# Kernel tuning notes

Hardware: AMD Instinct MI355X
Metric: run time of the kernel (lower is better)

Reference implementation:

```python
import jax, jax.numpy as jnp
import numpy as np

HID = 4096      # hidden_size
H = 32          # num_attention_heads
K = 8           # num_key_value_heads
D = HID // H    # head_dim = 128
G = H // K      # q heads per kv group = 4
INTER = 14336   # intermediate_size
T = 2048        # tokens (prefill)
EPS = 1e-5
THETA = 1000000.0


def setup_inputs() -> dict:
    key = jax.random.key(0)
    ks = jax.random.split(key, 9)
    s = 0.02
    return {
        "hidden_states": jax.random.normal(ks[0], (T, HID), jnp.float32),
        "position_ids": jnp.arange(T, dtype=jnp.int64),
        "wqkv": jax.random.normal(ks[1], ((H + 2 * K) * D, HID), jnp.float32) * s,
        "wo": jax.random.normal(ks[2], (HID, HID), jnp.float32) * s,
        "w1": jax.random.normal(ks[3], (INTER, HID), jnp.float32) * s,  # gate
        "w3": jax.random.normal(ks[4], (INTER, HID), jnp.float32) * s,  # up
        "w2": jax.random.normal(ks[5], (HID, INTER), jnp.float32) * s,  # down
        "attn_norm_w": jnp.ones((HID,), jnp.float32),
        "ffn_norm_w": jnp.ones((HID,), jnp.float32),
    }


def _rmsnorm(x, w):
    var = jnp.mean(jnp.square(x), axis=-1, keepdims=True)
    return x * jax.lax.rsqrt(var + EPS) * w


def _rope(x, cos, sin):
    # non-interleaved (half-split) rotation; x: [T, h, D], cos/sin: [T, 1, D//2]
    x1, x2 = x[..., : D // 2], x[..., D // 2 :]
    return jnp.concatenate([x1 * cos - x2 * sin, x2 * cos + x1 * sin], axis=-1)


def _attention(x, position_ids, wqkv, wo):
    t = x.shape[0]
    qkv = x @ wqkv.T  # [T, (H+2K)*D]
    q = qkv[:, : H * D].reshape(t, H, D)
    k = qkv[:, H * D : (H + K) * D].reshape(t, K, D)
    v = qkv[:, (H + K) * D :].reshape(t, K, D)

    inv_freq = 1.0 / (THETA ** (jnp.arange(0, D, 2, dtype=jnp.float32) / D))
    freqs = position_ids.astype(jnp.float32)[:, None] * inv_freq  # [T, D//2]
    cos = jnp.cos(freqs)[:, None, :]
    sin = jnp.sin(freqs)[:, None, :]
    q = _rope(q, cos, sin)
    k = _rope(k, cos, sin)

    # grouped-query attention: [T, K, G, D] queries vs [T, K, D] keys
    qg = q.reshape(t, K, G, D)
    scale = 1.0 / jnp.sqrt(jnp.float32(D))
    scores = jnp.einsum("tkgd,skd->kgts", qg, k) * scale  # [K, G, T, T]
    causal = jnp.tril(jnp.ones((t, t), dtype=bool))
    scores = jnp.where(causal, scores, jnp.finfo(scores.dtype).min)
    probs = jax.nn.softmax(scores, axis=-1)
    out = jnp.einsum("kgts,skd->tkgd", probs, v).reshape(t, H * D)
    return out @ wo.T


def _mlp(x, w1, w3, w2):
    return (jax.nn.silu(x @ w1.T) * (x @ w3.T)) @ w2.T


def reference(hidden_states, position_ids, wqkv, wo, w1, w3, w2, attn_norm_w, ffn_norm_w):
    h = hidden_states + _attention(_rmsnorm(hidden_states, attn_norm_w), position_ids, wqkv, wo)
    return h + _mlp(_rmsnorm(h, ffn_norm_w), w1, w3, w2)
```

## Files before the change

kernel.cpp:

```cpp
#include <hip/hip_runtime.h>
#include <stdint.h>

#define T_SEQ 2048
#define HIDN  4096
#define NH    32
#define NKV   8
#define DH    128
#define INTER 14336
#define QKV_N 6144
#define EPSR  1e-5f
#define SCALE 0.08838834764831845f
#define KVB   64

typedef __bf16 bf16x8 __attribute__((ext_vector_type(8)));
typedef float  f32x4  __attribute__((ext_vector_type(4)));

__device__ __forceinline__ f32x4 mfma16(bf16x8 a, bf16x8 b, f32x4 c) {
  return __builtin_amdgcn_mfma_f32_16x16x32_bf16(a, b, c, 0, 0, 0);
}

__device__ __forceinline__ void glds16(const void* g, void* l) {
  __builtin_amdgcn_global_load_lds(
      (__attribute__((address_space(1))) void*)g,
      (__attribute__((address_space(3))) void*)l,
      16, 0, 0);
}

__global__ __launch_bounds__(256) void cvt_all_kernel(
    const float* __restrict__ wqkv, const float* __restrict__ wo,
    const float* __restrict__ w1, const float* __restrict__ w3,
    const float* __restrict__ w2, __bf16* __restrict__ dst) {
  const long E0 = (long)QKV_N * HIDN;
  const long E1 = E0 + (long)HIDN * HIDN;
  const long E2 = E1 + 2L * INTER * HIDN;
  const long E3 = E2 + (long)HIDN * INTER;
  long stride = (long)gridDim.x * 256 * 16;
  for (long f = ((long)blockIdx.x * 256 + threadIdx.x) * 16; f < E3; f += stride) {
    const float* src;
    if (f < E0) {
      src = wqkv + f;
    } else if (f < E1) {
      src = wo + (f - E0);
    } else if (f < E2) {
      long l = f - E1;
      int c = (int)(l >> 12), i = (int)(l & 4095);
      int tau = c >> 8, j2 = c & 255;
      int wn = j2 >> 6, j = j2 & 63, nt = j >> 4, k16 = j & 15;
      src = (nt < 2 ? w1 : w3) +
            (size_t)(tau * 128 + wn * 32 + (nt & 1) * 16 + k16) * HIDN + i;
    } else {
      src = w2 + (f - E2);
    }
    float4 a = *(const float4*)(src);
    float4 b = *(const float4*)(src + 4);
    float4 e = *(const float4*)(src + 8);
    float4 g = *(const float4*)(src + 12);
    bf16x8 o0, o1;
    o0[0]=(__bf16)a.x; o0[1]=(__bf16)a.y; o0[2]=(__bf16)a.z; o0[3]=(__bf16)a.w;
    o0[4]=(__bf16)b.x; o0[5]=(__bf16)b.y; o0[6]=(__bf16)b.z; o0[7]=(__bf16)b.w;
    o1[0]=(__bf16)e.x; o1[1]=(__bf16)e.y; o1[2]=(__bf16)e.z; o1[3]=(__bf16)e.w;
    o1[4]=(__bf16)g.x; o1[5]=(__bf16)g.y; o1[6]=(__bf16)g.z; o1[7]=(__bf16)g.w;
    *(bf16x8*)(dst + f) = o0;
    *(bf16x8*)(dst + f + 8) = o1;
  }
}

__global__ __launch_bounds__(256) void rmsnorm_kernel(
    const float* __restrict__ x, const float* __restrict__ w,
    __bf16* __restrict__ y) {
  const int row = blockIdx.x, tid = threadIdx.x;
  const float* xr = x + (size_t)row * HIDN + tid * 16;
  float4 v0 = ((const float4*)xr)[0];
  float4 v1 = ((const float4*)xr)[1];
  float4 v2 = ((const float4*)xr)[2];
  float4 v3 = ((const float4*)xr)[3];
  float ss = v0.x*v0.x + v0.y*v0.y + v0.z*v0.z + v0.w*v0.w
           + v1.x*v1.x + v1.y*v1.y + v1.z*v1.z + v1.w*v1.w
           + v2.x*v2.x + v2.y*v2.y + v2.z*v2.z + v2.w*v2.w
           + v3.x*v3.x + v3.y*v3.y + v3.z*v3.z + v3.w*v3.w;
  #pragma unroll
  for (int off = 32; off >= 1; off >>= 1) ss += __shfl_xor(ss, off, 64);
  __shared__ float red[4];
  if ((tid & 63) == 0) red[tid >> 6] = ss;
  __syncthreads();
  float rn = rsqrtf((red[0] + red[1] + red[2] + red[3]) * (1.0f / HIDN) + EPSR);
  const float* wr = w + tid * 16;
  #pragma unroll
  for (int h = 0; h < 2; h++) {
    float4 a = ((const float4*)xr)[h*2], b = ((const float4*)xr)[h*2+1];
    float4 wa = ((const float4*)wr)[h*2], wb = ((const float4*)wr)[h*2+1];
    bf16x8 o;
    o[0]=(__bf16)(a.x*rn*wa.x); o[1]=(__bf16)(a.y*rn*wa.y);
    o[2]=(__bf16)(a.z*rn*wa.z); o[3]=(__bf16)(a.w*rn*wa.w);
    o[4]=(__bf16)(b.x*rn*wb.x); o[5]=(__bf16)(b.y*rn*wb.y);
    o[6]=(__bf16)(b.z*rn*wb.z); o[7]=(__bf16)(b.w*rn*wb.w);
    *(bf16x8*)(y + (size_t)row * HIDN + tid * 16 + h * 8) = o;
  }
}

__global__ __launch_bounds__(256) void add3_rms_kernel(
    const float* __restrict__ p, const float* __restrict__ resid,
    const float* __restrict__ w, float* __restrict__ hout,
    __bf16* __restrict__ xn) {
  const int row = blockIdx.x, tid = threadIdx.x;
  const size_t base = (size_t)row * HIDN + tid * 16;
  const size_t half = (size_t)T_SEQ * HIDN;
  float h[16];
  float ss = 0.f;
  #pragma unroll
  for (int q = 0; q < 4; q++) {
    float4 a = *(const float4*)(p + base + q * 4);
    float4 b = *(const float4*)(p + half + base + q * 4);
    float4 c = *(const float4*)(resid + base + q * 4);
    h[q*4+0] = a.x + b.x + c.x; h[q*4+1] = a.y + b.y + c.y;
    h[q*4+2] = a.z + b.z + c.z; h[q*4+3] = a.w + b.w + c.w;
    ss += h[q*4]*h[q*4] + h[q*4+1]*h[q*4+1] + h[q*4+2]*h[q*4+2] + h[q*4+3]*h[q*4+3];
    *(float4*)(hout + base + q * 4) = *(float4*)&h[q*4];
  }
  #pragma unroll
  for (int off = 32; off >= 1; off >>= 1) ss += __shfl_xor(ss, off, 64);
  __shared__ float red[4];
  if ((tid & 63) == 0) red[tid >> 6] = ss;
  __syncthreads();
  float rn = rsqrtf((red[0] + red[1] + red[2] + red[3]) * (1.0f / HIDN) + EPSR);
  #pragma unroll
  for (int hb = 0; hb < 2; hb++) {
    bf16x8 o;
    #pragma unroll
    for (int e = 0; e < 8; e++) {
      float wv = w[tid * 16 + hb * 8 + e];
      o[e] = (__bf16)(h[hb*8+e] * rn * wv);
    }
    *(bf16x8*)(xn + base + hb * 8) = o;
  }
}

template<int EPI>
__global__ __launch_bounds__(512, 2) void gemm256_kernel(
    const __bf16* __restrict__ A, const __bf16* __restrict__ B,
    void* __restrict__ Cout, int M, int N, int Kfull, int KZ, int Nout) {
  extern __shared__ __align__(16) char smem[];
  const int tid = threadIdx.x;
  const int lane = tid & 63;
  const int wv = tid >> 6;
  const int wm = wv >> 2;
  const int wn = wv & 3;
  const int lr = lane & 15, ql = lane >> 4;

  const int gx = gridDim.x, gy = gridDim.y;
  const int nwg = gx * gy;
  const int orig = blockIdx.y * gx + blockIdx.x;
  const int cpx = nwg >> 3;
  const int swz = (orig & 7) * cpx + (orig >> 3);
  const int by = swz % gy, bx = swz / gy;
  const int m0 = by * 256, n0 = bx * 256;
  const int kbase = blockIdx.z * KZ;
  const int NT = KZ >> 6;

  const int u0 = tid, u1 = tid + 512;
  const int r0 = u0 >> 2, r1 = u1 >> 2;
  const int p0 = (u0 & 3) ^ ((r0 >> 1) & 3);
  const int p1 = (u1 & 3) ^ ((r1 >> 1) & 3);
  const char* aR0 = (const char*)(A + (size_t)(m0 + r0) * Kfull + kbase) + p0 * 16;
  const char* aR1 = (const char*)(A + (size_t)(m0 + r1) * Kfull + kbase) + p1 * 16;
  const char* bR0 = (const char*)(B + (size_t)(n0 + r0) * Kfull + kbase) + p0 * 16;
  const char* bR1 = (const char*)(B + (size_t)(n0 + r1) * Kfull + kbase) + p1 * 16;
  const int d0 = u0 * 16, d1 = u1 * 16;

  const int sA = ql ^ ((lr >> 1) & 3);
  int aoff[8], boff[4];
  #pragma unroll
  for (int mt = 0; mt < 8; mt++) aoff[mt] = (wm * 128 + mt * 16 + lr) * 64 + sA * 16;
  #pragma unroll
  for (int nt = 0; nt < 4; nt++) boff[nt] = (wn * 64 + nt * 16 + lr) * 64 + sA * 16;

#define STAGE_A(t, kh, b) do {                                         \
    const size_t _o = (size_t)(t) * 128 + (kh) * 64;                   \
    glds16(aR0 + _o, smem + (b) * 65536 + (kh) * 16384 + d0);          \
    glds16(aR1 + _o, smem + (b) * 65536 + (kh) * 16384 + d1);          \
  } while (0)
#define STAGE_B(t, kh, b) do {                                         \
    const size_t _o = (size_t)(t) * 128 + (kh) * 64;                   \
    glds16(bR0 + _o, smem + (b) * 65536 + 32768 + (kh) * 16384 + d0);  \
    glds16(bR1 + _o, smem + (b) * 65536 + 32768 + (kh) * 16384 + d1);  \
  } while (0)
#define LDA4(dst, mb, b, ks) do {                                      \
    const char* _p = smem + (b) * 65536 + (ks) * 16384;                \
    dst[0] = *(const bf16x8*)(_p + aoff[(mb) + 0]);                    \
    dst[1] = *(const bf16x8*)(_p + aoff[(mb) + 1]);                    \
    dst[2] = *(const bf16x8*)(_p + aoff[(mb) + 2]);                    \
    dst[3] = *(const bf16x8*)(_p + aoff[(mb) + 3]);                    \
  } while (0)
#define LDB4(dst, b, ks) do {                                          \
    const char* _p = smem + (b) * 65536 + 32768 + (ks) * 16384;        \
    dst[0] = *(const bf16x8*)(_p + boff[0]);                           \
    dst[1] = *(const bf16x8*)(_p + boff[1]);                           \
    dst[2] = *(const bf16x8*)(_p + boff[2]);                           \
    dst[3] = *(const bf16x8*)(_p + boff[3]);                           \
  } while (0)
#define VMW(n)  asm volatile("s_waitcnt vmcnt(" #n ")" ::: "memory")
#define BAR()   __builtin_amdgcn_s_barrier()
#define LGKM(n) do { asm volatile("s_waitcnt lgkmcnt(" #n ")" ::: "memory"); \
    __builtin_amdgcn_sched_barrier(0); } while (0)
#define MFMA16(mb, AF, BF) do {                                        \
    __builtin_amdgcn_s_setprio(1);                                     \
    _Pragma("unroll") for (int _m = 0; _m < 4; _m++)                   \
      _Pragma("unroll") for (int _n = 0; _n < 4; _n++)                 \
        acc[(mb) + _m][_n] = mfma16(AF[_m], BF[_n], acc[(mb) + _m][_n]); \
    __builtin_amdgcn_s_setprio(0);                                     \
  } while (0)

  f32x4 acc[8][4] = {};
  bf16x8 af0[4], af1[4], bf0[4], bf1[4];

  STAGE_A(0, 0, 0); STAGE_B(0, 0, 0);
  STAGE_A(0, 1, 0); STAGE_B(0, 1, 0);
  STAGE_A(1, 0, 1); STAGE_B(1, 0, 1);
  VMW(8);
  BAR();
  LDA4(af0, 0, 0, 0); LDB4(bf0, 0, 0);

  const int NI = NT >> 1;
  for (int i = 0; i < NI - 1; ++i) {
    const int t1 = 2 * i + 1, s2 = 2 * i + 2, s3 = 2 * i + 3;
    LDA4(af1, 4, 0, 0);
    STAGE_A(t1, 1, 1);
    LGKM(4);
    MFMA16(0, af0, bf0);
    VMW(6); BAR();
    LDA4(af0, 0, 0, 1); LDB4(bf1, 0, 1);
    STAGE_B(t1, 1, 1);
    LGKM(8);
    MFMA16(4, af1, bf0);
    VMW(6); BAR();
    LDA4(af1, 4, 0, 1);
    STAGE_A(s2, 0, 0);
    LGKM(4);
    MFMA16(0, af0, bf1);
    VMW(6); BAR();
    LDA4(af0, 0, 1, 0); LDB4(bf0, 1, 0);
    STAGE_B(s2, 0, 0);
    LGKM(8);
    MFMA16(4, af1, bf1);
    VMW(6); BAR();
    LDA4(af1, 4, 1, 0);
    STAGE_A(s2, 1, 0);
    LGKM(4);
    MFMA16(0, af0, bf0);
    VMW(6); BAR();
    LDA4(af0, 0, 1, 1); LDB4(bf1, 1, 1);
    STAGE_B(s2, 1, 0);
    LGKM(8);
    MFMA16(4, af1, bf0);
    VMW(6); BAR();
    LDA4(af1, 4, 1, 1);
    STAGE_A(s3, 0, 1);
    LGKM(4);
    MFMA16(0, af0, bf1);
    VMW(6); BAR();
    LDA4(af0, 0, 0, 0); LDB4(bf0, 0, 0);
    STAGE_B(s3, 0, 1);
    LGKM(8);
    MFMA16(4, af1, bf1);
    VMW(6); BAR();
  }
  {
    const int t1 = NT - 1;
    LDA4(af1, 4, 0, 0);
    STAGE_A(t1, 1, 1);
    LGKM(4);
    MFMA16(0, af0, bf0);
    VMW(6); BAR();
    LDA4(af0, 0, 0, 1); LDB4(bf1, 0, 1);
    STAGE_B(t1, 1, 1);
    LGKM(8);
    MFMA16(4, af1, bf0);
    BAR();
    LDA4(af1, 4, 0, 1);
    LGKM(4);
    MFMA16(0, af0, bf1);
    VMW(2); BAR();
    LDA4(af0, 0, 1, 0); LDB4(bf0, 1, 0);
    LGKM(8);
    MFMA16(4, af1, bf1);
    BAR();
    LDA4(af1, 4, 1, 0);
    LGKM(4);
    MFMA16(0, af0, bf0);
    VMW(0); BAR();
    LDA4(af0, 0, 1, 1); LDB4(bf1, 1, 1);
    LGKM(8);
    MFMA16(4, af1, bf0);
    BAR();
    LDA4(af1, 4, 1, 1);
    LGKM(4);
    MFMA16(0, af0, bf1);
    BAR();
    LGKM(0);
    MFMA16(4, af1, bf1);
  }

#undef STAGE_A
#undef STAGE_B
#undef LDA4
#undef LDB4
#undef VMW
#undef BAR
#undef LGKM
#undef MFMA16

  #pragma unroll
  for (int mt = 0; mt < 8; mt++) {
    #pragma unroll
    for (int r = 0; r < 4; r++) {
      int rr = m0 + wm * 128 + mt * 16 + ql * 4 + r;
      if (EPI == 2) {
        #pragma unroll
        for (int nt = 0; nt < 2; nt++) {
          float u = acc[mt][nt][r];
          float v = acc[mt][nt + 2][r];
          float g = u / (1.0f + __expf(-u)) * v;
          int cc = (n0 >> 1) + wn * 32 + nt * 16 + lr;
          ((__bf16*)Cout)[(size_t)rr * Nout + cc] = (__bf16)g;
        }
      } else {
        #pragma unroll
        for (int nt = 0; nt < 4; nt++) {
          int cc = n0 + wn * 64 + nt * 16 + lr;
          size_t ix = (size_t)rr * N + cc;
          float val = acc[mt][nt][r];
          if (EPI == 0) ((float*)Cout)[(size_t)blockIdx.z * M * N + ix] = val;
          else          ((__bf16*)Cout)[ix] = (__bf16)val;
        }
      }
    }
  }
}

__global__ __launch_bounds__(256) void add3_kernel(
    const float* __restrict__ p, const float* __restrict__ r,
    float* __restrict__ o, long n) {
  long stride = (long)gridDim.x * 1024;
  for (long i = ((long)blockIdx.x * 256 + threadIdx.x) * 4; i < n; i += stride) {
    float4 a = *(const float4*)(p + i);
    float4 b = *(const float4*)(p + n + i);
    float4 c = *(const float4*)(r + i);
    float4 o4;
    o4.x = a.x + b.x + c.x; o4.y = a.y + b.y + c.y;
    o4.z = a.z + b.z + c.z; o4.w = a.w + b.w + c.w;
    *(float4*)(o + i) = o4;
  }
}

__global__ __launch_bounds__(256) void rope_vtrans_kernel(
    const __bf16* __restrict__ qkv, __bf16* __restrict__ q_r,
    __bf16* __restrict__ k_r, __bf16* __restrict__ v_t) {
  __shared__ float cs[64], sn[64];
  __shared__ __bf16 tile[64][136];
  const int tid = threadIdx.x;
  const int bid = blockIdx.x;
  if (bid < T_SEQ) {
    const int t = bid;
    if (tid < 64) {
      float inv = exp2f(-(float)tid * (19.931568569324174f / 64.0f));
      float f = (float)t * inv;
      cs[tid] = cosf(f);
      sn[tid] = sinf(f);
    }
    __syncthreads();
    const __bf16* row = qkv + (size_t)t * QKV_N;
    for (int it = tid; it < 40 * 64; it += 256) {
      int hh = it >> 6, i = it & 63;
      float x1 = (float)row[hh * 128 + i];
      float x2 = (float)row[hh * 128 + 64 + i];
      float c = cs[i], s = sn[i];
      float o1 = x1 * c - x2 * s;
      float o2 = x2 * c + x1 * s;
      if (hh < NH) {
        __bf16* qo = q_r + (size_t)t * HIDN + hh * 128;
        qo[i] = (__bf16)o1;
        qo[64 + i] = (__bf16)o2;
      } else {
        __bf16* ko = k_r + (size_t)t * (NKV * DH) + (hh - NH) * 128;
        ko[i] = (__bf16)o1;
        ko[64 + i] = (__bf16)o2;
      }
    }
  } else {
    const int b2 = bid - T_SEQ;
    const int t0 = (b2 & 31) * 64, kh = b2 >> 5;
    #pragma unroll
    for (int i = 0; i < 4; i++) {
      int u = i * 256 + tid;
      int row = u >> 4, c = (u & 15) * 8;
      *(bf16x8*)&tile[row][c] =
          *(const bf16x8*)(qkv + (size_t)(t0 + row) * QKV_N + (NH + NKV) * DH + kh * DH + c);
    }
    __syncthreads();
    const int d = tid & 127, th = (tid >> 7) * 32;
    #pragma unroll
    for (int j = 0; j < 4; j++) {
      int t = th + j * 8;
      bf16x8 o;
      #pragma unroll
      for (int e = 0; e < 8; e++) o[e] = tile[t + e][d];
      *(bf16x8*)(v_t + ((size_t)kh * DH + d) * T_SEQ + t0 + t) = o;
    }
  }
}

__global__ __launch_bounds__(256) void attn_kernel(
    const __bf16* __restrict__ q_r, const __bf16* __restrict__ k_r,
    const __bf16* __restrict__ v_t, __bf16* __restrict__ attn_o) {
  __shared__ __align__(16) __bf16 Ks[KVB * 128];
  __shared__ __align__(16) __bf16 Vs[128 * KVB];
  __shared__ __align__(16) __bf16 Pl[4 * 16 * KVB];

  const int tid = threadIdx.x;
  const int lane = tid & 63, wv = tid >> 6;
  const int lr = lane & 15, g = lane >> 4;
  const int qt = gridDim.x - 1 - blockIdx.x;
  const int h = blockIdx.y;
  const int kh = h >> 2;
  const int q0b = qt * 64;
  const int q0w = q0b + wv * 16;

  bf16x8 qf[4];
  {
    const __bf16* qp = q_r + (size_t)(q0w + lr) * HIDN + h * DH + g * 8;
    #pragma unroll
    for (int kk = 0; kk < 4; kk++) qf[kk] = *(const bf16x8*)(qp + kk * 32);
  }

  f32x4 o[8] = {};
  float mrun[4] = {-1e30f, -1e30f, -1e30f, -1e30f};
  float lrun[4] = {0.f, 0.f, 0.f, 0.f};
  char* PlW = (char*)Pl + wv * 2048;

  for (int kv0 = 0; kv0 < q0b + KVB; kv0 += KVB) {
    __syncthreads();
    #pragma unroll
    for (int i = 0; i < 4; i++) {
      int u = i * 256 + tid;
      int row = u >> 4;
      int cb = ((u & 15) * 16) ^ ((row & 7) << 4);
      glds16((const char*)(k_r + (size_t)(kv0 + row) * (NKV * DH) + kh * DH) + cb,
             (char*)Ks + u * 16);
    }
    #pragma unroll
    for (int i = 0; i < 4; i++) {
      int u = i * 256 + tid;
      int row = u >> 3;
      int cb = ((u & 7) * 16) ^ ((row & 7) << 4);
      glds16((const char*)(v_t + ((size_t)kh * DH + row) * T_SEQ + kv0) + cb,
             (char*)Vs + u * 16);
    }
    __syncthreads();

    if (q0w + 15 >= kv0) {
      f32x4 s[4] = {};
      #pragma unroll
      for (int kk = 0; kk < 4; kk++) {
        #pragma unroll
        for (int jt = 0; jt < 4; jt++) {
          int krow = jt * 16 + lr;
          int cb = (kk * 64 + g * 16) ^ ((krow & 7) << 4);
          bf16x8 kf = *(const bf16x8*)((char*)Ks + krow * 256 + cb);
          s[jt] = mfma16(qf[kk], kf, s[jt]);
        }
      }
      const bool need_mask = (kv0 + KVB - 1) > q0w;
      #pragma unroll
      for (int r = 0; r < 4; r++) {
        int qpos = q0w + g * 4 + r;
        int prow = g * 4 + r;
        float p[4];
        #pragma unroll
        for (int jt = 0; jt < 4; jt++) {
          float v = s[jt][r] * SCALE;
          if (need_mask && (kv0 + jt * 16 + lr > qpos)) v = -1e30f;
          p[jt] = v;
        }
        float mx = fmaxf(fmaxf(p[0], p[1]), fmaxf(p[2], p[3]));
        #pragma unroll
        for (int off = 1; off < 16; off <<= 1) mx = fmaxf(mx, __shfl_xor(mx, off, 64));
        float mn = fmaxf(mrun[r], mx);
        float corr = __expf(mrun[r] - mn);
        mrun[r] = mn;
        float ps = 0.f;
        #pragma unroll
        for (int jt = 0; jt < 4; jt++) {
          p[jt] = __expf(p[jt] - mn);
          ps += p[jt];
          int cbyte = ((jt * 16 + lr) * 2) ^ ((prow & 7) << 4);
          *(__bf16*)(PlW + prow * 128 + cbyte) = (__bf16)p[jt];
        }
        #pragma unroll
        for (int off = 1; off < 16; off <<= 1) ps += __shfl_xor(ps, off, 64);
        lrun[r] = lrun[r] * corr + ps;
        #pragma unroll
        for (int nt = 0; nt < 8; nt++) o[nt][r] *= corr;
      }
      bf16x8 pa[2];
      #pragma unroll
      for (int ks = 0; ks < 2; ks++)
        pa[ks] = *(const bf16x8*)(PlW + lr * 128 + ((g * 16 + ks * 64) ^ ((lr & 7) << 4)));
      #pragma unroll
      for (int nt = 0; nt < 8; nt++) {
        #pragma unroll
        for (int ks = 0; ks < 2; ks++) {
          int vrow = nt * 16 + lr;
          int cb = (ks * 64 + g * 16) ^ ((vrow & 7) << 4);
          bf16x8 vf = *(const bf16x8*)((char*)Vs + vrow * 128 + cb);
          o[nt] = mfma16(pa[ks], vf, o[nt]);
        }
      }
    }
  }

  #pragma unroll
  for (int nt = 0; nt < 8; nt++) {
    #pragma unroll
    for (int r = 0; r < 4; r++) {
      int qrow = q0w + g * 4 + r;
      int d = nt * 16 + lr;
      attn_o[(size_t)qrow * HIDN + h * DH + d] = (__bf16)(o[nt][r] / lrun[r]);
    }
  }
}

extern "C" void kernel_launch(void* const* d_in, const int* in_sizes, int n_in,
                              void* d_out, int out_size, void* d_ws, size_t ws_size,
                              hipStream_t stream) {
  const float* hidden = (const float*)d_in[0];
  const float* wqkv = (const float*)d_in[2];
  const float* wo   = (const float*)d_in[3];
  const float* w1   = (const float*)d_in[4];
  const float* w3   = (const float*)d_in[5];
  const float* w2   = (const float*)d_in[6];
  const float* anw  = (const float*)d_in[7];
  const float* fnw  = (const float*)d_in[8];

  char* ws = (char*)d_ws;
  const size_t SZ_XN   = (size_t)T_SEQ * HIDN * 2;
  const size_t SZ_QKV  = (size_t)T_SEQ * QKV_N * 2;
  const size_t SZ_KR   = (size_t)T_SEQ * NKV * DH * 2;
  const size_t SZ_H    = (size_t)T_SEQ * HIDN * 4;
  const size_t SZ_UV   = (size_t)T_SEQ * INTER * 2;

  const size_t W_QKV = (size_t)QKV_N * HIDN * 2;
  const size_t W_O   = (size_t)HIDN * HIDN * 2;
  const size_t W_I   = (size_t)INTER * HIDN * 2;
  const size_t W_TOTAL = W_QKV + W_O + 3 * W_I;

  char* act = ws + W_TOTAL;

  __bf16* xn1    = (__bf16*)(act);
  __bf16* qkv    = (__bf16*)(act + SZ_XN);
  __bf16* q_r    = (__bf16*)(act + SZ_XN + SZ_QKV);
  __bf16* gbuf   = (__bf16*)(act);
  __bf16* k_r    = (__bf16*)(act + SZ_UV);
  __bf16* attn_o = (__bf16*)(act + SZ_UV + SZ_KR);
  float*  hbuf   = (float*) (act + SZ_UV + SZ_KR + SZ_XN);
  __bf16* v_t    = (__bf16*)(act + SZ_UV + SZ_KR + SZ_XN);
  __bf16* xn2    = (__bf16*)(act + SZ_UV + SZ_KR + SZ_XN + SZ_H);
  float*  pbuf   = (float*)(act + SZ_UV + SZ_KR + SZ_XN + SZ_H + SZ_XN);

  __bf16* wall_b = (__bf16*)(ws);
  __bf16* wqkv_b = wall_b;
  __bf16* wo_b   = (__bf16*)(ws + W_QKV);
  __bf16* w13_b  = (__bf16*)(ws + W_QKV + W_O);
  __bf16* w2_b   = (__bf16*)(ws + W_QKV + W_O + 2 * W_I);

  const int LDS_BYTES = 131072;
  hipFuncSetAttribute((const void*)gemm256_kernel<0>,
                      hipFuncAttributeMaxDynamicSharedMemorySize, LDS_BYTES);
  hipFuncSetAttribute((const void*)gemm256_kernel<1>,
                      hipFuncAttributeMaxDynamicSharedMemorySize, LDS_BYTES);
  hipFuncSetAttribute((const void*)gemm256_kernel<2>,
                      hipFuncAttributeMaxDynamicSharedMemorySize, LDS_BYTES);

  cvt_all_kernel<<<2048, 256, 0, stream>>>(wqkv, wo, w1, w3, w2, wall_b);

  rmsnorm_kernel<<<T_SEQ, 256, 0, stream>>>(hidden, anw, xn1);
  gemm256_kernel<1><<<dim3(QKV_N / 256, T_SEQ / 256, 1), 512, LDS_BYTES, stream>>>(
      xn1, wqkv_b, qkv, T_SEQ, QKV_N, HIDN, HIDN, QKV_N);
  rope_vtrans_kernel<<<T_SEQ + 256, 256, 0, stream>>>(qkv, q_r, k_r, v_t);
  attn_kernel<<<dim3(T_SEQ / 64, NH), 256, 0, stream>>>(q_r, k_r, v_t, attn_o);
  gemm256_kernel<0><<<dim3(HIDN / 256, T_SEQ / 256, 2), 512, LDS_BYTES, stream>>>(
      attn_o, wo_b, pbuf, T_SEQ, HIDN, HIDN, HIDN / 2, HIDN);
  add3_rms_kernel<<<T_SEQ, 256, 0, stream>>>(pbuf, hidden, fnw, hbuf, xn2);
  gemm256_kernel<2><<<dim3(2 * INTER / 256, T_SEQ / 256, 1), 512, LDS_BYTES, stream>>>(
      xn2, w13_b, gbuf, T_SEQ, 2 * INTER, HIDN, HIDN, INTER);
  gemm256_kernel<0><<<dim3(HIDN / 256, T_SEQ / 256, 2), 512, LDS_BYTES, stream>>>(
      gbuf, w2_b, pbuf, T_SEQ, HIDN, INTER, INTER / 2, HIDN);
  add3_kernel<<<2048, 256, 0, stream>>>(pbuf, hbuf, (float*)d_out, (long)T_SEQ * HIDN);
}
```

Baseline: 1.278 ms.

## Restructure GEMM mainloop into five-stage ring of 32-wide K slices

```diff
diff --git a/kernel.cpp b/kernel.cpp
--- a/kernel.cpp
+++ b/kernel.cpp
@@ -155,7 +155,7 @@
   const int by = swz % gy, bx = swz / gy;
   const int m0 = by * 256, n0 = bx * 256;
   const int kbase = blockIdx.z * KZ;
-  const int NT = KZ >> 6;
+  const int NT = KZ >> 5;
 
   const int u0 = tid, u1 = tid + 512;
   const int r0 = u0 >> 2, r1 = u1 >> 2;
@@ -172,27 +172,25 @@
   #pragma unroll
   for (int mt = 0; mt < 8; mt++) aoff[mt] = (wm * 128 + mt * 16 + lr) * 64 + sA * 16;
   #pragma unroll
-  for (int nt = 0; nt < 4; nt++) boff[nt] = (wn * 64 + nt * 16 + lr) * 64 + sA * 16;
-
-#define STAGE_A(t, kh, b) do {                                         \
-    const size_t _o = (size_t)(t) * 128 + (kh) * 64;                   \
-    glds16(aR0 + _o, smem + (b) * 65536 + (kh) * 16384 + d0);          \
-    glds16(aR1 + _o, smem + (b) * 65536 + (kh) * 16384 + d1);          \
+  for (int nt = 0; nt < 4; nt++) boff[nt] = 16384 + (wn * 64 + nt * 16 + lr) * 64 + sA * 16;
+
+#define STAGE_AB(t, b) do {                                            \
+    const size_t _o = (size_t)(t) * 64;                                \
+    char* _d = smem + (b) * 32768;                                     \
+    glds16(aR0 + _o, _d + d0);                                         \
+    glds16(aR1 + _o, _d + d1);                                         \
+    glds16(bR0 + _o, _d + 16384 + d0);                                 \
+    glds16(bR1 + _o, _d + 16384 + d1);                                 \
   } while (0)
-#define STAGE_B(t, kh, b) do {                                         \
-    const size_t _o = (size_t)(t) * 128 + (kh) * 64;                   \
-    glds16(bR0 + _o, smem + (b) * 65536 + 32768 + (kh) * 16384 + d0);  \
-    glds16(bR1 + _o, smem + (b) * 65536 + 32768 + (kh) * 16384 + d1);  \
-  } while (0)
-#define LDA4(dst, mb, b, ks) do {                                      \
-    const char* _p = smem + (b) * 65536 + (ks) * 16384;                \
+#define LDA4(dst, mb, b) do {                                          \
+    const char* _p = smem + (b) * 32768;                               \
     dst[0] = *(const bf16x8*)(_p + aoff[(mb) + 0]);                    \
     dst[1] = *(const bf16x8*)(_p + aoff[(mb) + 1]);                    \
     dst[2] = *(const bf16x8*)(_p + aoff[(mb) + 2]);                    \
     dst[3] = *(const bf16x8*)(_p + aoff[(mb) + 3]);                    \
   } while (0)
-#define LDB4(dst, b, ks) do {                                          \
-    const char* _p = smem + (b) * 65536 + 32768 + (ks) * 16384;        \
+#define LDB4(dst, b) do {                                              \
+    const char* _p = smem + (b) * 32768;                               \
     dst[0] = *(const bf16x8*)(_p + boff[0]);                           \
     dst[1] = *(const bf16x8*)(_p + boff[1]);                           \
     dst[2] = *(const bf16x8*)(_p + boff[2]);                           \
@@ -209,105 +207,68 @@
         acc[(mb) + _m][_n] = mfma16(AF[_m], BF[_n], acc[(mb) + _m][_n]); \
     __builtin_amdgcn_s_setprio(0);                                     \
   } while (0)
+#define INC5(v) v = (v == 4) ? 0 : v + 1
 
   f32x4 acc[8][4] = {};
-  bf16x8 af0[4], af1[4], bf0[4], bf1[4];
-
-  STAGE_A(0, 0, 0); STAGE_B(0, 0, 0);
-  STAGE_A(0, 1, 0); STAGE_B(0, 1, 0);
-  STAGE_A(1, 0, 1); STAGE_B(1, 0, 1);
-  VMW(8);
+  bf16x8 af0E[4], af0O[4], af1[4], bfE[4], bfO[4];
+
+  STAGE_AB(0, 0); STAGE_AB(1, 1); STAGE_AB(2, 2); STAGE_AB(3, 3);
+  VMW(12);
   BAR();
-  LDA4(af0, 0, 0, 0); LDB4(bf0, 0, 0);
-
-  const int NI = NT >> 1;
-  for (int i = 0; i < NI - 1; ++i) {
-    const int t1 = 2 * i + 1, s2 = 2 * i + 2, s3 = 2 * i + 3;
-    LDA4(af1, 4, 0, 0);
-    STAGE_A(t1, 1, 1);
+  LDA4(af0E, 0, 0); LDB4(bfE, 0);
+
+  int bc = 0, bn = 1, sb = 4;
+  for (int t = 0; t < NT - 4; t += 2) {
+    LDA4(af1, 4, bc);
+    STAGE_AB(t + 4, sb);
     LGKM(4);
-    MFMA16(0, af0, bf0);
-    VMW(6); BAR();
-    LDA4(af0, 0, 0, 1); LDB4(bf1, 0, 1);
-    STAGE_B(t1, 1, 1);
+    MFMA16(0, af0E, bfE);
+    BAR();
+    LDA4(af0O, 0, bn); LDB4(bfO, bn);
     LGKM(8);
-    MFMA16(4, af1, bf0);
-    VMW(6); BAR();
-    LDA4(af1, 4, 0, 1);
-    STAGE_A(s2, 0, 0);
+    MFMA16(4, af1, bfE);
+    VMW(8); BAR();
+    bc = bn; INC5(bn); INC5(sb);
+    LDA4(af1, 4, bc);
+    STAGE_AB(t + 5, sb);
     LGKM(4);
-    MFMA16(0, af0, bf1);
-    VMW(6); BAR();
-    LDA4(af0, 0, 1, 0); LDB4(bf0, 1, 0);
-    STAGE_B(s2, 0, 0);
+    MFMA16(0, af0O, bfO);
+    BAR();
+    LDA4(af0E, 0, bn); LDB4(bfE, bn);
     LGKM(8);
-    MFMA16(4, af1, bf1);
-    VMW(6); BAR();
-    LDA4(af1, 4, 1, 0);
-    STAGE_A(s2, 1, 0);
-    LGKM(4);
-    MFMA16(0, af0, bf0);
-    VMW(6); BAR();
-    LDA4(af0, 0, 1, 1); LDB4(bf1, 1, 1);
-    STAGE_B(s2, 1, 0);
-    LGKM(8);
-    MFMA16(4, af1, bf0);
-    VMW(6); BAR();
-    LDA4(af1, 4, 1, 1);
-    STAGE_A(s3, 0, 1);
-    LGKM(4);
-    MFMA16(0, af0, bf1);
-    VMW(6); BAR();
-    LDA4(af0, 0, 0, 0); LDB4(bf0, 0, 0);
-    STAGE_B(s3, 0, 1);
-    LGKM(8);
-    MFMA16(4, af1, bf1);
-    VMW(6); BAR();
-  }
-  {
-    const int t1 = NT - 1;
-    LDA4(af1, 4, 0, 0);
-    STAGE_A(t1, 1, 1);
-    LGKM(4);
-    MFMA16(0, af0, bf0);
-    VMW(6); BAR();
-    LDA4(af0, 0, 0, 1); LDB4(bf1, 0, 1);
-    STAGE_B(t1, 1, 1);
-    LGKM(8);
-    MFMA16(4, af1, bf0);
-    BAR();
-    LDA4(af1, 4, 0, 1);
-    LGKM(4);
-    MFMA16(0, af0, bf1);
-    VMW(2); BAR();
-    LDA4(af0, 0, 1, 0); LDB4(bf0, 1, 0);
-    LGKM(8);
-    MFMA16(4, af1, bf1);
-    BAR();
-    LDA4(af1, 4, 1, 0);
-    LGKM(4);
-    MFMA16(0, af0, bf0);
-    VMW(0); BAR();
-    LDA4(af0, 0, 1, 1); LDB4(bf1, 1, 1);
-    LGKM(8);
-    MFMA16(4, af1, bf0);
-    BAR();
-    LDA4(af1, 4, 1, 1);
-    LGKM(4);
-    MFMA16(0, af0, bf1);
-    BAR();
-    LGKM(0);
-    MFMA16(4, af1, bf1);
-  }
-
-#undef STAGE_A
-#undef STAGE_B
+    MFMA16(4, af1, bfO);
+    VMW(8); BAR();
+    bc = bn; INC5(bn); INC5(sb);
+  }
+  LDA4(af1, 4, bc);
+  LGKM(4); MFMA16(0, af0E, bfE); BAR();
+  LDA4(af0O, 0, bn); LDB4(bfO, bn);
+  LGKM(8); MFMA16(4, af1, bfE);
+  VMW(4); BAR();
+  bc = bn; INC5(bn);
+  LDA4(af1, 4, bc);
+  LGKM(4); MFMA16(0, af0O, bfO); BAR();
+  LDA4(af0E, 0, bn); LDB4(bfE, bn);
+  LGKM(8); MFMA16(4, af1, bfO);
+  VMW(0); BAR();
+  bc = bn; INC5(bn);
+  LDA4(af1, 4, bc);
+  LGKM(4); MFMA16(0, af0E, bfE); BAR();
+  LDA4(af0O, 0, bn); LDB4(bfO, bn);
+  LGKM(8); MFMA16(4, af1, bfE); BAR();
+  bc = bn;
+  LDA4(af1, 4, bc);
+  LGKM(4); MFMA16(0, af0O, bfO); BAR();
+  LGKM(0); MFMA16(4, af1, bfO);
+
+#undef STAGE_AB
 #undef LDA4
 #undef LDB4
 #undef VMW
 #undef BAR
 #undef LGKM
 #undef MFMA16
+#undef INC5
 
   #pragma unroll
   for (int mt = 0; mt < 8; mt++) {
@@ -572,7 +533,7 @@
   __bf16* w13_b  = (__bf16*)(ws + W_QKV + W_O);
   __bf16* w2_b   = (__bf16*)(ws + W_QKV + W_O + 2 * W_I);
 
-  const int LDS_BYTES = 131072;
+  const int LDS_BYTES = 163840;
   hipFuncSetAttribute((const void*)gemm256_kernel<0>,
                       hipFuncAttributeMaxDynamicSharedMemorySize, LDS_BYTES);
   hipFuncSetAttribute((const void*)gemm256_kernel<1>,
```

Result: slower. 1.303 ms (+2.0%).
